# Kernel optimization log

Hardware: AMD Instinct MI355X
Metric: run time of the kernel (lower is better)

Reference implementation:

```python
import jax, jax.numpy as jnp
import numpy as np

BETA = 0.25  # commitment/codebook mixing as in VQVAE.__init__


def setup_inputs() -> dict:
    key = jax.random.key(0)
    k1, k2 = jax.random.split(key)
    # z: encoder latent [B, C, H, W] with C = latent_dim
    z = jax.random.normal(k1, (32, 64, 64, 64), dtype=jnp.float32)
    # codebook: nn.Embedding(num_embeddings, latent_dim).weight
    codebook = jax.random.normal(k2, (1024, 64), dtype=jnp.float32)
    return {"z": z, "codebook": codebook}


def reference(z, codebook):
    B, C, H, W = z.shape
    zf = z.reshape(B, C, H * W).transpose(0, 2, 1)  # [B, N, C], N = H*W
    # Squared Euclidean distances; argmin identical to torch.cdist(p=2) argmin
    # since sqrt is monotone (min_distances are unused in the original forward).
    d2 = (jnp.sum(zf * zf, axis=-1, keepdims=True)              # [B, N, 1]
          + jnp.sum(codebook * codebook, axis=-1)[None, None, :]  # [1, 1, K]
          - 2.0 * jnp.einsum('bnc,kc->bnk', zf, codebook))        # [B, N, K]
    indices = jnp.argmin(d2, axis=-1)                            # [B, N]
    z_q = codebook[indices]                                      # [B, N, C] gather
    z_q = z_q.transpose(0, 2, 1).reshape(B, C, H, W)
    commitment_loss = jnp.mean((jax.lax.stop_gradient(z_q) - z) ** 2)
    codebook_loss = jnp.mean((z_q - jax.lax.stop_gradient(z)) ** 2)
    loss = commitment_loss + BETA * codebook_loss
    return z_q, loss
```

## Files before the change

### kernel.cpp

```cpp
#include <hip/hip_runtime.h>
#include <float.h>

#define HW    4096
#define NC    64
#define NK    1024
#define NB    32
#define NPIX  (NB*HW)
#define TOTAL (NPIX*NC)
#define PPB   256

#define MARGIN 8e-3f

typedef __attribute__((ext_vector_type(8))) short short8;
typedef __attribute__((ext_vector_type(4))) float floatx4;

__device__ __forceinline__ unsigned short f2bf(float f) {
    unsigned u = __float_as_uint(f);
    u += 0x7FFFu + ((u >> 16) & 1u);
    return (unsigned short)(u >> 16);
}
__device__ __forceinline__ float bf2f(unsigned short h) {
    return __uint_as_float(((unsigned)h) << 16);
}

__global__ void vq_prep_kernel(const float* __restrict__ cb,
                               float* __restrict__ cnorm,
                               unsigned short* __restrict__ cb_hi,
                               unsigned short* __restrict__ cb_lo,
                               float* __restrict__ loss_out) {
    const int b = blockIdx.x;
    if (b < 64) {
        const int i = b * 256 + threadIdx.x;
        if (i == 0) loss_out[0] = 0.0f;
        float4 v = ((const float4*)cb)[i];
        unsigned short h0 = f2bf(v.x), h1 = f2bf(v.y),
                       h2 = f2bf(v.z), h3 = f2bf(v.w);
        unsigned short l0 = f2bf(v.x - bf2f(h0)), l1 = f2bf(v.y - bf2f(h1)),
                       l2 = f2bf(v.z - bf2f(h2)), l3 = f2bf(v.w - bf2f(h3));
        uint2 ph = make_uint2((unsigned)h0 | ((unsigned)h1 << 16),
                              (unsigned)h2 | ((unsigned)h3 << 16));
        uint2 pl = make_uint2((unsigned)l0 | ((unsigned)l1 << 16),
                              (unsigned)l2 | ((unsigned)l3 << 16));
        ((uint2*)cb_hi)[i] = ph;
        ((uint2*)cb_lo)[i] = pl;
    } else {
        const int k = (b - 64) * 256 + threadIdx.x;
        const float4* r4 = (const float4*)(cb + (size_t)k * NC);
        double s = 0.0;
        #pragma unroll
        for (int j = 0; j < 16; ++j) {
            float4 v = r4[j];
            s = fma((double)v.x, (double)v.x, s);
            s = fma((double)v.y, (double)v.y, s);
            s = fma((double)v.z, (double)v.z, s);
            s = fma((double)v.w, (double)v.w, s);
        }
        cnorm[k] = (float)s;
    }
}

__global__ __launch_bounds__(256, 4) void vq_mfma_kernel(
        const float* __restrict__ z,
        const float* __restrict__ cb,
        const unsigned short* __restrict__ cb_hi,
        const unsigned short* __restrict__ cb_lo,
        const float* __restrict__ cnorm,
        float* __restrict__ zq,
        float* __restrict__ loss_out) {
    __shared__ alignas(16) char smem[32768];
    __shared__ alignas(16) float cn_lds[NK];
    __shared__ int   finidx[PPB];
    __shared__ int   flags[PPB];
    __shared__ float redf[4];

    const int tid = threadIdx.x;
    const int g0  = blockIdx.x * PPB;
    const int bb  = g0 >> 12;
    const int pp0 = g0 & 4095;
    const float* zbase = z  + (size_t)bb * (NC * HW) + pp0;
    float*      zqbase = zq + (size_t)bb * (NC * HW) + pp0;

    ((float4*)cn_lds)[tid] = ((const float4*)cnorm)[tid];

    const int lane = tid & 63;
    const int w    = tid >> 6;
    const int q    = lane >> 4;
    const int pcol = lane & 15;

    unsigned short (*zh)[PPB] = (unsigned short(*)[PPB])smem;
    unsigned short (*zl)[PPB] = (unsigned short(*)[PPB])(smem + 16384);

    short8 Bh[2][4], Bl[2][4];
    #pragma unroll
    for (int r = 0; r < 2; ++r) {
        const int px4 = (tid & 63) * 4;
        const int c0  = tid >> 6;
        #pragma unroll
        for (int it = 0; it < 8; ++it) {
            const int c = it * 4 + c0;
            float4 v = *(const float4*)(zbase + (size_t)(r * 32 + c) * HW + px4);
            v.x *= -2.0f; v.y *= -2.0f; v.z *= -2.0f; v.w *= -2.0f;
            unsigned short h0 = f2bf(v.x), h1 = f2bf(v.y),
                           h2 = f2bf(v.z), h3 = f2bf(v.w);
            unsigned short l0 = f2bf(v.x - bf2f(h0)), l1 = f2bf(v.y - bf2f(h1)),
                           l2 = f2bf(v.z - bf2f(h2)), l3 = f2bf(v.w - bf2f(h3));
            uint2 ph = make_uint2((unsigned)h0 | ((unsigned)h1 << 16),
                                  (unsigned)h2 | ((unsigned)h3 << 16));
            uint2 pl = make_uint2((unsigned)l0 | ((unsigned)l1 << 16),
                                  (unsigned)l2 | ((unsigned)l3 << 16));
            *(uint2*)&zh[c][px4] = ph;
            *(uint2*)&zl[c][px4] = pl;
        }
        __syncthreads();
        #pragma unroll
        for (int j = 0; j < 4; ++j) {
            const int px = w * 64 + j * 16 + pcol;
            #pragma unroll
            for (int t = 0; t < 8; ++t) {
                Bh[r][j][t] = (short)zh[q * 8 + t][px];
                Bl[r][j][t] = (short)zl[q * 8 + t][px];
            }
        }
        __syncthreads();
    }

    uint4* abuf = (uint4*)smem;
    const int spart = tid >> 7;
    const int sidx  = tid & 127;
    const int srow  = sidx >> 3;
    const int schk  = sidx & 7;
    const int ldst  = spart * 128 + srow * 8 + (schk ^ (srow & 7));
    const char* gsrc = (spart == 0 ? (const char*)cb_hi : (const char*)cb_lo)
                       + (size_t)sidx * 16;

    const int ridx0 = pcol * 8 + (q ^ (pcol & 7));
    const int ridx1 = pcol * 8 + ((4 + q) ^ (pcol & 7));

    uint4 sreg = *(const uint4*)(gsrc);
    abuf[ldst] = sreg;
    sreg = *(const uint4*)(gsrc + 2048);
    __syncthreads();

    float B1[4] = {FLT_MAX, FLT_MAX, FLT_MAX, FLT_MAX};
    float B2[4] = {FLT_MAX, FLT_MAX, FLT_MAX, FLT_MAX};
    int   I1[4] = {0, 0, 0, 0};

    #pragma unroll 2
    for (int tile = 0; tile < 64; ++tile) {
        if (tile < 63) abuf[((tile + 1) & 1) * 256 + ldst] = sreg;
        if (tile < 62) sreg = *(const uint4*)(gsrc + (size_t)(tile + 2) * 2048);

        const short8* A = (const short8*)smem + (tile & 1) * 256;
        short8 ah0 = A[ridx0];
        short8 ah1 = A[ridx1];
        short8 al0 = A[128 + ridx0];
        short8 al1 = A[128 + ridx1];

        const floatx4 cn4 = *(const floatx4*)&cn_lds[tile * 16 + q * 4];
        const int kb = tile * 16 + q * 4;
        #pragma unroll
        for (int j = 0; j < 4; ++j) {
            floatx4 a0 = __builtin_amdgcn_mfma_f32_16x16x32_bf16(ah0, Bh[0][j], cn4, 0, 0, 0);
            floatx4 a1 = {0.f, 0.f, 0.f, 0.f};
            a1 = __builtin_amdgcn_mfma_f32_16x16x32_bf16(ah1, Bh[1][j], a1, 0, 0, 0);
            a0 = __builtin_amdgcn_mfma_f32_16x16x32_bf16(ah0, Bl[0][j], a0, 0, 0, 0);
            a1 = __builtin_amdgcn_mfma_f32_16x16x32_bf16(ah1, Bl[1][j], a1, 0, 0, 0);
            a0 = __builtin_amdgcn_mfma_f32_16x16x32_bf16(al0, Bh[0][j], a0, 0, 0, 0);
            a1 = __builtin_amdgcn_mfma_f32_16x16x32_bf16(al1, Bh[1][j], a1, 0, 0, 0);

            #pragma unroll
            for (int i = 0; i < 4; ++i) {
                float s = a0[i] + a1[i];
                bool lt = s < B1[j];
                I1[j] = lt ? (kb + i) : I1[j];
                B2[j] = __builtin_amdgcn_fmed3f(s, B1[j], B2[j]);
                B1[j] = fminf(s, B1[j]);
            }
        }
        __syncthreads();
    }

    #pragma unroll
    for (int j = 0; j < 4; ++j) {
        float b1 = B1[j], b2 = B2[j];
        int i1 = I1[j];
        #pragma unroll
        for (int d = 16; d <= 32; d <<= 1) {
            float ob1 = __shfl_xor(b1, d);
            float ob2 = __shfl_xor(b2, d);
            int   oi1 = __shfl_xor(i1, d);
            float nb2 = fminf(fmaxf(b1, ob1), fminf(b2, ob2));
            bool lt = (ob1 < b1) || (ob1 == b1 && oi1 < i1);
            b1 = lt ? ob1 : b1;
            i1 = lt ? oi1 : i1;
            b2 = nb2;
        }
        if (q == 0) {
            const int px = w * 64 + j * 16 + pcol;
            finidx[px] = i1;
            flags[px]  = (b2 - b1 < MARGIN) ? 1 : 0;
        }
    }
    int myflag = 0;
    __syncthreads();
    myflag = flags[tid];
    const int nflag = __syncthreads_count(myflag);

    if (nflag > 0) {
        double* red_s = reinterpret_cast<double*>(cn_lds);
        int*    red_i = reinterpret_cast<int*>(cn_lds + 512);
        for (int p = 0; p < PPB; ++p) {
            if (flags[p]) {
                const float* zp = zbase + p;
                double bd = 1.0e300; int bi = 0;
                #pragma unroll 1
                for (int r = 0; r < 4; ++r) {
                    const int k = tid * 4 + r;
                    const float* rowp = cb + (size_t)k * NC;
                    double s = 0.0;
                    for (int c = 0; c < NC; ++c) {
                        double t = (double)zp[(size_t)c * HW] - (double)rowp[c];
                        s = fma(t, t, s);
                    }
                    if (s < bd) { bd = s; bi = k; }
                }
                red_s[tid] = bd; red_i[tid] = bi;
                __syncthreads();
                if (tid < 64) {
                    double m = red_s[tid]; int mi = red_i[tid];
                    #pragma unroll
                    for (int t = 1; t < 4; ++t) {
                        double om = red_s[tid + 64 * t];
                        int    oi = red_i[tid + 64 * t];
                        if (om < m || (om == m && oi < mi)) { m = om; mi = oi; }
                    }
                    #pragma unroll
                    for (int off = 32; off > 0; off >>= 1) {
                        double om = __shfl_down(m, off);
                        int    oi = __shfl_down(mi, off);
                        if (om < m || (om == m && oi < mi)) { m = om; mi = oi; }
                    }
                    if (tid == 0) finidx[p] = mi;
                }
                __syncthreads();
            }
        }
        __syncthreads();
    }

    {
        const int p  = tid;
        const int fi = finidx[p];
        const float4* crow4 = (const float4*)(cb + (size_t)fi * NC);
        float sse = 0.f;
        #pragma unroll
        for (int j = 0; j < 16; ++j) {
            const float4 qv = crow4[j];
            const size_t c0 = (size_t)(4 * j) * HW + p;
            const float z0 = zbase[c0];
            const float z1 = zbase[c0 + HW];
            const float z2 = zbase[c0 + 2 * (size_t)HW];
            const float z3 = zbase[c0 + 3 * (size_t)HW];
            zqbase[c0]                  = qv.x;
            zqbase[c0 + HW]             = qv.y;
            zqbase[c0 + 2 * (size_t)HW] = qv.z;
            zqbase[c0 + 3 * (size_t)HW] = qv.w;
            float t0 = qv.x - z0, t1 = qv.y - z1, t2 = qv.z - z2, t3 = qv.w - z3;
            sse = fmaf(t0, t0, sse);
            sse = fmaf(t1, t1, sse);
            sse = fmaf(t2, t2, sse);
            sse = fmaf(t3, t3, sse);
        }
        #pragma unroll
        for (int off = 32; off > 0; off >>= 1) sse += __shfl_down(sse, off);
        if ((tid & 63) == 0) redf[tid >> 6] = sse;
        __syncthreads();
        if (tid == 0)
            atomicAdd(loss_out, (redf[0] + redf[1] + redf[2] + redf[3]) *
                                (1.25f / (float)TOTAL));
    }
}

extern "C" void kernel_launch(void* const* d_in, const int* in_sizes, int n_in,
                              void* d_out, int out_size, void* d_ws, size_t ws_size,
                              hipStream_t stream) {
    const float* z  = (const float*)d_in[0];
    const float* cb = (const float*)d_in[1];
    float* out      = (float*)d_out;
    float* zqp      = out;
    float* loss     = out + TOTAL;

    float* cnorm          = (float*)d_ws;
    unsigned short* cb_hi = (unsigned short*)((char*)d_ws + 4096);
    unsigned short* cb_lo = (unsigned short*)((char*)d_ws + 4096 + NK * NC * 2);

    vq_prep_kernel<<<68, 256, 0, stream>>>(cb, cnorm, cb_hi, cb_lo, loss);
    vq_mfma_kernel<<<NPIX / PPB, 256, 0, stream>>>(z, cb, cb_hi, cb_lo, cnorm,
                                                   zqp, loss);
}
```

Measured before the change: 216.5 us.

## Halve pixels per block and load z fragments directly into registers

Cuts pixels per block from 256 to 128, so each wave holds two 16-pixel fragments instead of four. The z operands are read from global memory straight into registers and split into bf16 hi/lo there, which removes the LDS staging buffer and two barriers. The epilogue splits channels between the two thread halves. This doubles the grid and lowers register and LDS pressure for better occupancy. In exchange, each block streams the whole codebook for half as many pixels, so codebook traffic per pixel doubles, and the uncoalesced strided z loads may cost more.

```diff
diff --git a/kernel.cpp b/kernel.cpp
--- a/kernel.cpp
+++ b/kernel.cpp
@@ -7,7 +7,7 @@
 #define NB    32
 #define NPIX  (NB*HW)
 #define TOTAL (NPIX*NC)
-#define PPB   256
+#define PPB   128
 
 #define MARGIN 8e-3f
 
@@ -67,7 +67,7 @@
         const float* __restrict__ cnorm,
         float* __restrict__ zq,
         float* __restrict__ loss_out) {
-    __shared__ alignas(16) char smem[32768];
+    __shared__ alignas(16) uint4 abuf[512];
     __shared__ alignas(16) float cn_lds[NK];
     __shared__ int   finidx[PPB];
     __shared__ int   flags[PPB];
@@ -87,44 +87,29 @@
     const int q    = lane >> 4;
     const int pcol = lane & 15;
 
-    unsigned short (*zh)[PPB] = (unsigned short(*)[PPB])smem;
-    unsigned short (*zl)[PPB] = (unsigned short(*)[PPB])(smem + 16384);
-
-    short8 Bh[2][4], Bl[2][4];
+    float zraw[2][2][8];
     #pragma unroll
-    for (int r = 0; r < 2; ++r) {
-        const int px4 = (tid & 63) * 4;
-        const int c0  = tid >> 6;
-        #pragma unroll
-        for (int it = 0; it < 8; ++it) {
-            const int c = it * 4 + c0;
-            float4 v = *(const float4*)(zbase + (size_t)(r * 32 + c) * HW + px4);
-            v.x *= -2.0f; v.y *= -2.0f; v.z *= -2.0f; v.w *= -2.0f;
-            unsigned short h0 = f2bf(v.x), h1 = f2bf(v.y),
-                           h2 = f2bf(v.z), h3 = f2bf(v.w);
-            unsigned short l0 = f2bf(v.x - bf2f(h0)), l1 = f2bf(v.y - bf2f(h1)),
-                           l2 = f2bf(v.z - bf2f(h2)), l3 = f2bf(v.w - bf2f(h3));
-            uint2 ph = make_uint2((unsigned)h0 | ((unsigned)h1 << 16),
-                                  (unsigned)h2 | ((unsigned)h3 << 16));
-            uint2 pl = make_uint2((unsigned)l0 | ((unsigned)l1 << 16),
-                                  (unsigned)l2 | ((unsigned)l3 << 16));
-            *(uint2*)&zh[c][px4] = ph;
-            *(uint2*)&zl[c][px4] = pl;
-        }
-        __syncthreads();
-        #pragma unroll
-        for (int j = 0; j < 4; ++j) {
-            const int px = w * 64 + j * 16 + pcol;
+    for (int ks = 0; ks < 2; ++ks)
+        #pragma unroll
+        for (int j = 0; j < 2; ++j)
+            #pragma unroll
+            for (int t = 0; t < 8; ++t)
+                zraw[ks][j][t] = zbase[(size_t)(ks * 32 + q * 8 + t) * HW
+                                       + (w * 32 + j * 16 + pcol)];
+    short8 Bh[2][2], Bl[2][2];
+    #pragma unroll
+    for (int ks = 0; ks < 2; ++ks)
+        #pragma unroll
+        for (int j = 0; j < 2; ++j)
             #pragma unroll
             for (int t = 0; t < 8; ++t) {
-                Bh[r][j][t] = (short)zh[q * 8 + t][px];
-                Bl[r][j][t] = (short)zl[q * 8 + t][px];
+                float v = -2.0f * zraw[ks][j][t];
+                unsigned short h = f2bf(v);
+                unsigned short l = f2bf(v - bf2f(h));
+                Bh[ks][j][t] = (short)h;
+                Bl[ks][j][t] = (short)l;
             }
-        }
-        __syncthreads();
-    }
-
-    uint4* abuf = (uint4*)smem;
+
     const int spart = tid >> 7;
     const int sidx  = tid & 127;
     const int srow  = sidx >> 3;
@@ -141,16 +126,16 @@
     sreg = *(const uint4*)(gsrc + 2048);
     __syncthreads();
 
-    float B1[4] = {FLT_MAX, FLT_MAX, FLT_MAX, FLT_MAX};
-    float B2[4] = {FLT_MAX, FLT_MAX, FLT_MAX, FLT_MAX};
-    int   I1[4] = {0, 0, 0, 0};
+    float B1[2] = {FLT_MAX, FLT_MAX};
+    float B2[2] = {FLT_MAX, FLT_MAX};
+    int   I1[2] = {0, 0};
 
     #pragma unroll 2
     for (int tile = 0; tile < 64; ++tile) {
         if (tile < 63) abuf[((tile + 1) & 1) * 256 + ldst] = sreg;
         if (tile < 62) sreg = *(const uint4*)(gsrc + (size_t)(tile + 2) * 2048);
 
-        const short8* A = (const short8*)smem + (tile & 1) * 256;
+        const short8* A = (const short8*)abuf + (tile & 1) * 256;
         short8 ah0 = A[ridx0];
         short8 ah1 = A[ridx1];
         short8 al0 = A[128 + ridx0];
@@ -159,7 +144,7 @@
         const floatx4 cn4 = *(const floatx4*)&cn_lds[tile * 16 + q * 4];
         const int kb = tile * 16 + q * 4;
         #pragma unroll
-        for (int j = 0; j < 4; ++j) {
+        for (int j = 0; j < 2; ++j) {
             floatx4 a0 = __builtin_amdgcn_mfma_f32_16x16x32_bf16(ah0, Bh[0][j], cn4, 0, 0, 0);
             floatx4 a1 = {0.f, 0.f, 0.f, 0.f};
             a1 = __builtin_amdgcn_mfma_f32_16x16x32_bf16(ah1, Bh[1][j], a1, 0, 0, 0);
@@ -181,7 +166,7 @@
     }
 
     #pragma unroll
-    for (int j = 0; j < 4; ++j) {
+    for (int j = 0; j < 2; ++j) {
         float b1 = B1[j], b2 = B2[j];
         int i1 = I1[j];
         #pragma unroll
@@ -196,14 +181,14 @@
             b2 = nb2;
         }
         if (q == 0) {
-            const int px = w * 64 + j * 16 + pcol;
+            const int px = w * 32 + j * 16 + pcol;
             finidx[px] = i1;
             flags[px]  = (b2 - b1 < MARGIN) ? 1 : 0;
         }
     }
     int myflag = 0;
     __syncthreads();
-    myflag = flags[tid];
+    if (tid < PPB) myflag = flags[tid];
     const int nflag = __syncthreads_count(myflag);
 
     if (nflag > 0) {
@@ -249,14 +234,15 @@
     }
 
     {
-        const int p  = tid;
+        const int p  = tid & (PPB - 1);
+        const int qq = tid >> 7;
         const int fi = finidx[p];
-        const float4* crow4 = (const float4*)(cb + (size_t)fi * NC);
+        const float4* crow4 = (const float4*)(cb + (size_t)fi * NC) + qq * 8;
         float sse = 0.f;
         #pragma unroll
-        for (int j = 0; j < 16; ++j) {
+        for (int j = 0; j < 8; ++j) {
             const float4 qv = crow4[j];
-            const size_t c0 = (size_t)(4 * j) * HW + p;
+            const size_t c0 = (size_t)(qq * 32 + 4 * j) * HW + p;
             const float z0 = zbase[c0];
             const float z1 = zbase[c0 + HW];
             const float z2 = zbase[c0 + 2 * (size_t)HW];
```

After: 176.6 us. -18.4%, faster.
